# Performance work log

Hardware: AMD Instinct MI355X
Metric: run time of the kernel (lower is better)

## Reference

```python
import jax, jax.numpy as jnp
import numpy as np
import math

B, T, E, H = 2, 2048, 1024, 16
HD = E // H


def layernorm(x, g, b, eps=1e-5):
    mu = jnp.mean(x, axis=-1, keepdims=True)
    var = jnp.var(x, axis=-1, keepdims=True)
    return (x - mu) * jax.lax.rsqrt(var + eps) * g + b


def new_gelu(x):
    c = math.sqrt(2.0 / math.pi)
    return 0.5 * x * (1.0 + jnp.tanh(c * (x + 0.044715 * x ** 3)))


def setup_inputs() -> dict:
    key = jax.random.key(0)
    ks = jax.random.split(key, 6)
    s = 0.02
    return {
        "x": jax.random.normal(ks[0], (B, T, E), jnp.float32),
        "ln1_g": jnp.ones((E,), jnp.float32),
        "ln1_b": jnp.zeros((E,), jnp.float32),
        "w_attn": jax.random.normal(ks[1], (E, 3 * E), jnp.float32) * s,
        "b_attn": jnp.zeros((3 * E,), jnp.float32),
        "w_proj": jax.random.normal(ks[2], (E, E), jnp.float32) * s,
        "b_proj": jnp.zeros((E,), jnp.float32),
        "ln2_g": jnp.ones((E,), jnp.float32),
        "ln2_b": jnp.zeros((E,), jnp.float32),
        "w_fc": jax.random.normal(ks[3], (E, 4 * E), jnp.float32) * s,
        "b_fc": jnp.zeros((4 * E,), jnp.float32),
        "w_fc2": jax.random.normal(ks[4], (4 * E, E), jnp.float32) * s,
        "b_fc2": jnp.zeros((E,), jnp.float32),
    }


def reference(x, ln1_g, ln1_b, w_attn, b_attn, w_proj, b_proj,
              ln2_g, ln2_b, w_fc, b_fc, w_fc2, b_fc2):
    # --- attention branch (pre-norm) ---
    h = layernorm(x, ln1_g, ln1_b)
    qkv = h @ w_attn + b_attn                      # [B,T,3E]
    q, k, v = jnp.split(qkv, 3, axis=-1)
    # [B,T,E] -> [B,H,T,HD]
    q = q.reshape(B, T, H, HD).transpose(0, 2, 1, 3)
    k = k.reshape(B, T, H, HD).transpose(0, 2, 1, 3)
    v = v.reshape(B, T, H, HD).transpose(0, 2, 1, 3)
    att = jnp.einsum('bhqd,bhkd->bhqk', q, k) * (1.0 / math.sqrt(HD))
    causal = jnp.tril(jnp.ones((T, T), bool))       # [T,T]
    att = jnp.where(causal, att, -jnp.inf)
    att = jax.nn.softmax(att, axis=-1)
    y = jnp.einsum('bhqk,bhkd->bhqd', att, v)       # [B,H,T,HD]
    y = y.transpose(0, 2, 1, 3).reshape(B, T, E)
    y = y @ w_proj + b_proj
    x = x + y
    # --- MLP branch (pre-norm) ---
    h = layernorm(x, ln2_g, ln2_b)
    h = new_gelu(h @ w_fc + b_fc)
    h = h @ w_fc2 + b_fc2
    return x + h
```

## Files before the change

kernel.cpp:

```cpp
#include <hip/hip_runtime.h>

typedef unsigned short u16;
typedef unsigned int   u32;
typedef short bf16x8 __attribute__((ext_vector_type(8)));
typedef float f32x4  __attribute__((ext_vector_type(4)));

__device__ __forceinline__ float bf_lo(u32 u){ return __uint_as_float(u << 16); }
__device__ __forceinline__ float bf_hi(u32 u){ return __uint_as_float(u & 0xffff0000u); }
__device__ __forceinline__ u16 bf16r(float f){
  u32 u = __float_as_uint(f);
  u += 0x7fffu + ((u >> 16) & 1u);
  return (u16)(u >> 16);
}
__device__ __forceinline__ u32 pack2(float a, float b){
  return (u32)bf16r(a) | ((u32)bf16r(b) << 16);
}
__device__ __forceinline__ u32 pk_trunc(float a, float b){
  return (__float_as_uint(a) >> 16) | (__float_as_uint(b) & 0xffff0000u);
}
__device__ __forceinline__ float gelu_f(float x){
  float t = 0.7978845608028654f * (x + 0.044715f * x * x * x);
  t = fminf(fmaxf(t, -12.f), 12.f);
  float e = __expf(2.f * t);
  float th = (e - 1.f) / (e + 1.f);
  return 0.5f * x * (1.f + th);
}
__device__ __forceinline__ void glds16(const void* g, void* l) {
  __builtin_amdgcn_global_load_lds(
      (const __attribute__((address_space(1))) void*)g,
      (__attribute__((address_space(3))) void*)l, 16, 0, 0);
}

#define QSCALE 0.1803368801111204f

__device__ __forceinline__ void wt_body(const float* __restrict__ W,
                                        u16* __restrict__ Wt, int K, int N,
                                        int kx, int nx) {
  __shared__ float t[32][33];
  int k0 = kx * 32, n0 = nx * 32;
  int tx = threadIdx.x & 31, ty = threadIdx.x >> 5;
  #pragma unroll
  for (int i = 0; i < 32; i += 8)
    t[ty + i][tx] = W[(size_t)(k0 + ty + i) * N + n0 + tx];
  __syncthreads();
  #pragma unroll
  for (int i = 0; i < 32; i += 8)
    Wt[(size_t)(n0 + ty + i) * K + k0 + tx] = bf16r(t[tx][ty + i]);
}

__device__ __forceinline__ void ln_body(const float* __restrict__ x,
                                        const float* __restrict__ g,
                                        const float* __restrict__ bta,
                                        u16* __restrict__ out, int row) {
  int tid = threadIdx.x;
  const float4 xv = ((const float4*)(x + (size_t)row * 1024))[tid];
  float s = xv.x + xv.y + xv.z + xv.w;
  float q = xv.x*xv.x + xv.y*xv.y + xv.z*xv.z + xv.w*xv.w;
  #pragma unroll
  for (int off = 32; off > 0; off >>= 1) {
    s += __shfl_down(s, off);
    q += __shfl_down(q, off);
  }
  __shared__ float ss[4], sq[4];
  if ((tid & 63) == 0) { ss[tid >> 6] = s; sq[tid >> 6] = q; }
  __syncthreads();
  s = ss[0] + ss[1] + ss[2] + ss[3];
  q = sq[0] + sq[1] + sq[2] + sq[3];
  float mu = s * (1.f/1024.f);
  float rs = rsqrtf(q * (1.f/1024.f) - mu*mu + 1e-5f);
  const float4 gv = ((const float4*)g)[tid];
  const float4 bv = ((const float4*)bta)[tid];
  uint2 o;
  o.x = pack2((xv.x-mu)*rs*gv.x + bv.x, (xv.y-mu)*rs*gv.y + bv.y);
  o.y = pack2((xv.z-mu)*rs*gv.z + bv.z, (xv.w-mu)*rs*gv.w + bv.w);
  ((uint2*)(out + (size_t)row * 1024))[tid] = o;
}

__global__ __launch_bounds__(256) void prep_k(
    const float* __restrict__ w_attn, const float* __restrict__ w_proj,
    const float* __restrict__ w_fc,   const float* __restrict__ w_fc2,
    u16* __restrict__ wt_attn, u16* __restrict__ wt_proj,
    u16* __restrict__ wt_fc,   u16* __restrict__ wt_fc2,
    const float* __restrict__ x, const float* __restrict__ g,
    const float* __restrict__ b, u16* __restrict__ h1)
{
  int i = blockIdx.x;
  if (i < 3072)       wt_body(w_attn, wt_attn, 1024, 3072, i & 31, i >> 5);
  else if (i < 4096)  { int j = i - 3072; wt_body(w_proj, wt_proj, 1024, 1024, j & 31, j >> 5); }
  else if (i < 8192)  { int j = i - 4096; wt_body(w_fc,   wt_fc,   1024, 4096, j & 31, j >> 5); }
  else if (i < 12288) { int j = i - 8192; wt_body(w_fc2,  wt_fc2,  4096, 1024, j & 127, j >> 7); }
  else                ln_body(x, g, b, h1, i - 12288);
}

__global__ __launch_bounds__(256) void ln_k(const float* __restrict__ x,
                                            const float* __restrict__ g,
                                            const float* __restrict__ bta,
                                            u16* __restrict__ out) {
  ln_body(x, g, bta, out, blockIdx.x);
}

template<int MODE, int MI, int LB>
__global__ __launch_bounds__(256, LB) void gemm_k(
    const u16* __restrict__ A, const u16* __restrict__ Bt,
    const float* __restrict__ bias, const float* __restrict__ resid,
    void* __restrict__ out, int M, int N, int K, int lda,
    u16* __restrict__ vtb)
{
  constexpr int TM = MI * 32;
  __shared__ u16 Al[TM * 64];
  __shared__ u16 Bl[128 * 64];
  const int tid = threadIdx.x;
  const int by = blockIdx.y;
  const int sp = (MODE == 5) ? (by >> 3) : 0;
  const int n0 = (MODE == 5) ? ((by & 7) * 128) : (by * 128);
  const size_t koff = (size_t)sp * K;
  const int m0 = blockIdx.x * TM;
  const int wave = tid >> 6, lane = tid & 63;
  const int wm = (wave >> 1) * (MI * 16), wn = (wave & 1) * 64;
  const int l15 = lane & 15, quad = lane >> 4;
  const int sr = lane >> 3, cs = lane & 7;
  f32x4 acc[MI][4];
  const f32x4 zero = {0.f, 0.f, 0.f, 0.f};
  #pragma unroll
  for (int i = 0; i < MI; ++i)
    #pragma unroll
    for (int j = 0; j < 4; ++j)
      acc[i][j] = zero;
  for (int k0 = 0; k0 < K; k0 += 64) {
    __syncthreads();
    #pragma unroll
    for (int it = 0; it < MI; ++it) {
      int r = it*32 + wave*8 + sr;
      int c = cs ^ (r & 7);
      glds16(&A[(size_t)(m0 + r) * lda + koff + k0 + c*8], &Al[(it*32 + wave*8) * 64]);
    }
    #pragma unroll
    for (int it = 0; it < 4; ++it) {
      int r = it*32 + wave*8 + sr;
      int c = cs ^ (r & 7);
      glds16(&Bt[(size_t)(n0 + r) * lda + koff + k0 + c*8], &Bl[(it*32 + wave*8) * 64]);
    }
    __syncthreads();
    #pragma unroll
    for (int kk = 0; kk < 2; ++kk) {
      bf16x8 af[MI], bfr[4];
      #pragma unroll
      for (int i = 0; i < MI; ++i) {
        int R = wm + i*16 + l15;
        af[i] = *(const bf16x8*)&Al[R*64 + ((kk*4 + quad) ^ (R & 7)) * 8];
      }
      #pragma unroll
      for (int j = 0; j < 4; ++j) {
        int R = wn + j*16 + l15;
        bfr[j] = *(const bf16x8*)&Bl[R*64 + ((kk*4 + quad) ^ (R & 7)) * 8];
      }
      #pragma unroll
      for (int i = 0; i < MI; ++i)
        #pragma unroll
        for (int j = 0; j < 4; ++j)
          acc[i][j] = __builtin_amdgcn_mfma_f32_16x16x32_bf16(af[i], bfr[j], acc[i][j], 0, 0, 0);
    }
  }
  #pragma unroll
  for (int i = 0; i < MI; ++i) {
    #pragma unroll
    for (int j = 0; j < 4; ++j) {
      int col = n0 + wn + j*16 + l15;
      float bv = (MODE == 5) ? 0.f : bias[col];
      if constexpr (MODE == 4) {
        if (col >= 2048) {
          int t0 = m0 + wm + i*16 + quad*4;
          size_t vidx = ((size_t)((t0 >> 11)*1024 + (col - 2048)))*2048 + (t0 & 2047);
          uint2 pw;
          pw.x = pack2(acc[i][j][0] + bv, acc[i][j][1] + bv);
          pw.y = pack2(acc[i][j][2] + bv, acc[i][j][3] + bv);
          *(uint2*)&vtb[vidx] = pw;
          continue;
        }
      }
      float sc = (MODE == 4 && col < 1024) ? QSCALE : 1.0f;
      #pragma unroll
      for (int r = 0; r < 4; ++r) {
        int row = m0 + wm + i*16 + quad*4 + r;
        size_t idx = (size_t)row * N + col;
        float v = acc[i][j][r] + bv;
        if constexpr (MODE == 0)      ((u16*)out)[idx] = bf16r(v);
        else if constexpr (MODE == 1) ((float*)out)[idx] = v + resid[idx];
        else if constexpr (MODE == 2) ((u16*)out)[idx] = bf16r(gelu_f(v));
        else if constexpr (MODE == 4) ((u16*)out)[idx] = bf16r(v * sc);
        else if constexpr (MODE == 5) ((u16*)out)[(size_t)sp*M*N + idx] = bf16r(v);
        else                          ((float*)out)[idx] = v + resid[idx];
      }
    }
  }
}

__global__ __launch_bounds__(256) void cmb_k(const u16* __restrict__ p,
                                             const float* __restrict__ bias,
                                             const float* __restrict__ x2,
                                             float* __restrict__ out) {
  int row = blockIdx.x, t = threadIdx.x;
  size_t i = (size_t)row * 1024 + t*4;
  uint2 a = *(const uint2*)&p[i];
  uint2 b = *(const uint2*)&p[4194304 + i];
  float4 xv = ((const float4*)x2)[i >> 2];
  float4 bv = ((const float4*)bias)[t];
  float4 o;
  o.x = bf_lo(a.x) + bf_lo(b.x) + bv.x + xv.x;
  o.y = bf_hi(a.x) + bf_hi(b.x) + bv.y + xv.y;
  o.z = bf_lo(a.y) + bf_lo(b.y) + bv.z + xv.z;
  o.w = bf_hi(a.y) + bf_hi(b.y) + bv.w + xv.w;
  ((float4*)out)[i >> 2] = o;
}

__global__ __launch_bounds__(256, 4) void attn_k(const u16* __restrict__ qkv,
                                                 const u16* __restrict__ Vt,
                                                 u16* __restrict__ y) {
  __shared__ u16 Kl[64*64];
  __shared__ u16 Vl[64*64];
  __shared__ u16 Pw[4*16*72];
  const int tid = threadIdx.x;
  const int bh = blockIdx.x & 31, bb = bh >> 4, h = bh & 15;
  const int qt = 31 - (int)(blockIdx.x >> 5);
  const int w = tid >> 6, lane = tid & 63;
  const int l15 = lane & 15, quad = lane >> 4;
  const int sr = lane >> 3, cs = lane & 7;
  u16* Pme = Pw + w * (16*72);
  const int w16l = w*16 + l15;
  const int dquad = quad*4;

  const u16* qp = qkv + ((size_t)(bb*2048 + qt*64 + w16l))*3072 + h*64 + quad*8;
  const bf16x8 aq0 = *(const bf16x8*)qp;
  const bf16x8 aq1 = *(const bf16x8*)(qp + 32);

  f32x4 o[4];
  const f32x4 zero = {0.f,0.f,0.f,0.f};
  #pragma unroll
  for (int dt = 0; dt < 4; ++dt) o[dt] = zero;
  float l = 0.f;

  const u16* kbase = qkv + (size_t)bb*2048*3072 + 1024 + h*64;
  const u16* vbase = Vt + (size_t)bh*64*2048;

  for (int kt = 0; kt <= qt; ++kt) {
    __syncthreads();
    #pragma unroll
    for (int it = 0; it < 2; ++it) {
      int r = it*32 + w*8 + sr;
      int c = cs ^ (r & 7);
      glds16(kbase + (size_t)(kt*64 + r)*3072 + c*8, &Kl[(it*32 + w*8) * 64]);
      glds16(vbase + (size_t)r*2048 + kt*64 + c*8,   &Vl[(it*32 + w*8) * 64]);
    }
    __syncthreads();
    bf16x8 ak[4][2], av[4][2];
    #pragma unroll
    for (int nt = 0; nt < 4; ++nt) {
      int R = nt*16 + l15;
      #pragma unroll
      for (int kk = 0; kk < 2; ++kk) {
        ak[nt][kk] = *(const bf16x8*)&Kl[R*64 + ((kk*4 + quad) ^ (R & 7)) * 8];
        av[nt][kk] = *(const bf16x8*)&Vl[R*64 + ((kk*4 + quad) ^ (R & 7)) * 8];
      }
    }
    f32x4 sv[4];
    #pragma unroll
    for (int nt = 0; nt < 4; ++nt) {
      f32x4 s = zero;
      s = __builtin_amdgcn_mfma_f32_16x16x32_bf16(ak[nt][0], aq0, s, 0, 0, 0);
      s = __builtin_amdgcn_mfma_f32_16x16x32_bf16(ak[nt][1], aq1, s, 0, 0, 0);
      sv[nt] = s;
    }
    if (kt == qt) {
      #pragma unroll
      for (int nt = 0; nt < 4; ++nt)
        #pragma unroll
        for (int r = 0; r < 4; ++r)
          if (nt*16 + dquad + r > w16l) sv[nt][r] = -1e30f;
    }
    float pv[4][4];
    #pragma unroll
    for (int nt = 0; nt < 4; ++nt)
      #pragma unroll
      for (int r = 0; r < 4; ++r)
        pv[nt][r] = exp2f(sv[nt][r]);
    l += ((pv[0][0]+pv[0][1])+(pv[0][2]+pv[0][3]))
       + ((pv[1][0]+pv[1][1])+(pv[1][2]+pv[1][3]))
       + ((pv[2][0]+pv[2][1])+(pv[2][2]+pv[2][3]))
       + ((pv[3][0]+pv[3][1])+(pv[3][2]+pv[3][3]));
    #pragma unroll
    for (int nt = 0; nt < 4; ++nt) {
      uint2 pr;
      pr.x = pk_trunc(pv[nt][0], pv[nt][1]);
      pr.y = pk_trunc(pv[nt][2], pv[nt][3]);
      *(uint2*)&Pme[l15*72 + nt*16 + dquad] = pr;
    }
    const bf16x8 bp0 = *(const bf16x8*)&Pme[l15*72 + quad*8];
    const bf16x8 bp1 = *(const bf16x8*)&Pme[l15*72 + 32 + quad*8];
    #pragma unroll
    for (int dt = 0; dt < 4; ++dt) {
      o[dt] = __builtin_amdgcn_mfma_f32_16x16x32_bf16(av[dt][0], bp0, o[dt], 0, 0, 0);
      o[dt] = __builtin_amdgcn_mfma_f32_16x16x32_bf16(av[dt][1], bp1, o[dt], 0, 0, 0);
    }
  }
  float lt = l;
  lt += __shfl_xor(lt, 16);
  lt += __shfl_xor(lt, 32);
  float inv = 1.f / lt;
  u16* yp = y + ((size_t)(bb*2048 + qt*64 + w16l))*1024 + h*64;
  #pragma unroll
  for (int dt = 0; dt < 4; ++dt) {
    uint2 pk;
    pk.x = pack2(o[dt][0]*inv, o[dt][1]*inv);
    pk.y = pack2(o[dt][2]*inv, o[dt][3]*inv);
    *(uint2*)(yp + dt*16 + dquad) = pk;
  }
}

extern "C" void kernel_launch(void* const* d_in, const int* in_sizes, int n_in,
                              void* d_out, int out_size, void* d_ws, size_t ws_size,
                              hipStream_t stream) {
  const float* x      = (const float*)d_in[0];
  const float* ln1_g  = (const float*)d_in[1];
  const float* ln1_b  = (const float*)d_in[2];
  const float* w_attn = (const float*)d_in[3];
  const float* b_attn = (const float*)d_in[4];
  const float* w_proj = (const float*)d_in[5];
  const float* b_proj = (const float*)d_in[6];
  const float* ln2_g  = (const float*)d_in[7];
  const float* ln2_b  = (const float*)d_in[8];
  const float* w_fc   = (const float*)d_in[9];
  const float* b_fc   = (const float*)d_in[10];
  const float* w_fc2  = (const float*)d_in[11];
  const float* b_fc2  = (const float*)d_in[12];

  char* ws = (char*)d_ws;
  u16*   wt_attn = (u16*)(ws);
  u16*   wt_proj = (u16*)(ws + 6291456);
  u16*   wt_fc   = (u16*)(ws + 8388608);
  u16*   wt_fc2  = (u16*)(ws + 16777216);
  u16*   h1      = (u16*)(ws + 25165824);
  u16*   qkvb    = (u16*)(ws + 33554432);
  u16*   yb      = (u16*)(ws + 58720256);
  float* x2      = (float*)(ws + 67108864);
  u16*   h2  = h1;
  u16*   vtb = (u16*)(ws + 67108864);
  u16*   act = qkvb;
  u16*   pk2 = (u16*)(ws);

  prep_k<<<dim3(16384), 256, 0, stream>>>(w_attn, w_proj, w_fc, w_fc2,
                                          wt_attn, wt_proj, wt_fc, wt_fc2,
                                          x, ln1_g, ln1_b, h1);
  gemm_k<4,4,3><<<dim3(32, 24), 256, 0, stream>>>(h1, wt_attn, b_attn, nullptr,
      (void*)qkvb, 4096, 3072, 1024, 1024, vtb);
  attn_k<<<dim3(1024), 256, 0, stream>>>(qkvb, vtb, yb);
  gemm_k<1,2,3><<<dim3(64, 8), 256, 0, stream>>>(yb, wt_proj, b_proj, x,
      (void*)x2, 4096, 1024, 1024, 1024, nullptr);
  ln_k<<<4096, 256, 0, stream>>>(x2, ln2_g, ln2_b, h2);
  gemm_k<2,4,3><<<dim3(32, 32), 256, 0, stream>>>(h2, wt_fc, b_fc, nullptr,
      (void*)act, 4096, 4096, 1024, 1024, nullptr);
  gemm_k<5,2,3><<<dim3(64, 16), 256, 0, stream>>>(act, wt_fc2, b_fc2, nullptr,
      (void*)pk2, 4096, 1024, 2048, 4096, nullptr);
  cmb_k<<<4096, 256, 0, stream>>>(pk2, b_fc2, x2, (float*)d_out);
}
```

Measured before the change: 311.3 us.

## Add 256x256 8-wave ping-pong GEMM kernel for QKV and FC1

```diff
diff --git a/kernel.cpp b/kernel.cpp
--- a/kernel.cpp
+++ b/kernel.cpp
@@ -167,18 +167,6 @@
     for (int j = 0; j < 4; ++j) {
       int col = n0 + wn + j*16 + l15;
       float bv = (MODE == 5) ? 0.f : bias[col];
-      if constexpr (MODE == 4) {
-        if (col >= 2048) {
-          int t0 = m0 + wm + i*16 + quad*4;
-          size_t vidx = ((size_t)((t0 >> 11)*1024 + (col - 2048)))*2048 + (t0 & 2047);
-          uint2 pw;
-          pw.x = pack2(acc[i][j][0] + bv, acc[i][j][1] + bv);
-          pw.y = pack2(acc[i][j][2] + bv, acc[i][j][3] + bv);
-          *(uint2*)&vtb[vidx] = pw;
-          continue;
-        }
-      }
-      float sc = (MODE == 4 && col < 1024) ? QSCALE : 1.0f;
       #pragma unroll
       for (int r = 0; r < 4; ++r) {
         int row = m0 + wm + i*16 + quad*4 + r;
@@ -187,12 +175,140 @@
         if constexpr (MODE == 0)      ((u16*)out)[idx] = bf16r(v);
         else if constexpr (MODE == 1) ((float*)out)[idx] = v + resid[idx];
         else if constexpr (MODE == 2) ((u16*)out)[idx] = bf16r(gelu_f(v));
-        else if constexpr (MODE == 4) ((u16*)out)[idx] = bf16r(v * sc);
         else if constexpr (MODE == 5) ((u16*)out)[(size_t)sp*M*N + idx] = bf16r(v);
         else                          ((float*)out)[idx] = v + resid[idx];
       }
     }
   }
+}
+
+#define BAR8 __builtin_amdgcn_s_barrier()
+#define VM4  asm volatile("s_waitcnt vmcnt(4)" ::: "memory")
+
+template<int MODE>
+__global__ __launch_bounds__(512, 2) void gemm8_k(
+    const u16* __restrict__ A, const u16* __restrict__ Bt,
+    const float* __restrict__ bias, void* __restrict__ out,
+    int M, int N, int K, int lda, u16* __restrict__ vtb)
+{
+  __shared__ u16 Al[2][256*64];
+  __shared__ u16 Bl[2][256*64];
+  const int tid = threadIdx.x;
+  const int m0 = blockIdx.x * 256;
+  const int n0 = blockIdx.y * 256;
+  const int wave = tid >> 6, lane = tid & 63;
+  const int wm = wave >> 2, wn = wave & 3;
+  const int l15 = lane & 15, quad = lane >> 4;
+  const int srow = tid >> 3;
+  const int scl  = (tid & 7) ^ (srow & 7);
+  const int NT = K >> 6;
+
+  const u16* pA = A  + (size_t)(m0 + srow) * lda + scl * 8;
+  const u16* pB = Bt + (size_t)(n0 + srow) * lda + scl * 8;
+
+  f32x4 acc[2][2][4][2];
+  const f32x4 zero = {0.f,0.f,0.f,0.f};
+  #pragma unroll
+  for (int a = 0; a < 2; ++a)
+    #pragma unroll
+    for (int b = 0; b < 2; ++b)
+      #pragma unroll
+      for (int c = 0; c < 4; ++c)
+        #pragma unroll
+        for (int d = 0; d < 2; ++d) acc[a][b][c][d] = zero;
+
+  bf16x8 afr[4][2];
+  bf16x8 bfr[2][2][2];
+
+#define STG_A(b,h,t) do { \
+    glds16(pA + ((h)*128      ) * lda + (t)*64, &Al[b][((h)*128      + wave*8) * 64]); \
+    glds16(pA + ((h)*128 + 64 ) * lda + (t)*64, &Al[b][((h)*128 + 64 + wave*8) * 64]); } while(0)
+#define STG_B(b,h,t) do { \
+    glds16(pB + ((h)*128      ) * lda + (t)*64, &Bl[b][((h)*128      + wave*8) * 64]); \
+    glds16(pB + ((h)*128 + 64 ) * lda + (t)*64, &Bl[b][((h)*128 + 64 + wave*8) * 64]); } while(0)
+#define RD_A(b,qm) do { _Pragma("unroll") \
+    for (int mi = 0; mi < 4; ++mi) { \
+      int R = (qm)*128 + wm*64 + mi*16 + l15; \
+      afr[mi][0] = *(const bf16x8*)&Al[b][R*64 + ((quad     ^ (l15 & 7)) * 8)]; \
+      afr[mi][1] = *(const bf16x8*)&Al[b][R*64 + (((4+quad) ^ (l15 & 7)) * 8)]; } } while(0)
+#define RD_B(b,qn) do { _Pragma("unroll") \
+    for (int ni = 0; ni < 2; ++ni) { \
+      int R = (qn)*128 + wn*32 + ni*16 + l15; \
+      bfr[qn][ni][0] = *(const bf16x8*)&Bl[b][R*64 + ((quad     ^ (l15 & 7)) * 8)]; \
+      bfr[qn][ni][1] = *(const bf16x8*)&Bl[b][R*64 + (((4+quad) ^ (l15 & 7)) * 8)]; } } while(0)
+#define MM(qm,qn) do { __builtin_amdgcn_s_setprio(1); _Pragma("unroll") \
+    for (int mi = 0; mi < 4; ++mi) { _Pragma("unroll") \
+      for (int ni = 0; ni < 2; ++ni) { \
+        acc[qm][qn][mi][ni] = __builtin_amdgcn_mfma_f32_16x16x32_bf16(afr[mi][0], bfr[qn][ni][0], acc[qm][qn][mi][ni], 0, 0, 0); \
+        acc[qm][qn][mi][ni] = __builtin_amdgcn_mfma_f32_16x16x32_bf16(afr[mi][1], bfr[qn][ni][1], acc[qm][qn][mi][ni], 0, 0, 0); } } \
+    __builtin_amdgcn_s_setprio(0); } while(0)
+
+  STG_A(0,0,0); STG_B(0,0,0); STG_A(0,1,0); STG_B(0,1,0);
+  STG_A(1,0,1); STG_B(1,0,1);
+  VM4; BAR8;
+
+  const int NI = NT >> 1;
+  for (int j = 0; j < NI; ++j) {
+    const int t1 = 2*j + 1;
+    const int t2 = (2*j + 2 < NT) ? 2*j + 2 : NT - 1;
+    const int t3 = (2*j + 3 < NT) ? 2*j + 3 : NT - 1;
+    RD_A(0,0); RD_B(0,0); STG_A(1,1,t1);
+    BAR8; MM(0,0); BAR8;
+    RD_B(0,1); STG_B(1,1,t1);
+    BAR8; MM(0,1); BAR8;
+    RD_A(0,1); STG_A(0,0,t2);
+    BAR8; MM(1,0); BAR8;
+    STG_B(0,0,t2);
+    BAR8; MM(1,1); VM4; BAR8;
+    RD_A(1,0); RD_B(1,0); STG_A(0,1,t2);
+    BAR8; MM(0,0); BAR8;
+    RD_B(1,1); STG_B(0,1,t2);
+    BAR8; MM(0,1); BAR8;
+    RD_A(1,1); STG_A(1,0,t3);
+    BAR8; MM(1,0); BAR8;
+    STG_B(1,0,t3);
+    BAR8; MM(1,1); VM4; BAR8;
+  }
+
+  #pragma unroll
+  for (int qm = 0; qm < 2; ++qm) {
+    #pragma unroll
+    for (int qn = 0; qn < 2; ++qn) {
+      #pragma unroll
+      for (int mi = 0; mi < 4; ++mi) {
+        #pragma unroll
+        for (int ni = 0; ni < 2; ++ni) {
+          const int col  = n0 + qn*128 + wn*32 + ni*16 + l15;
+          const int rowb = m0 + qm*128 + wm*64 + mi*16 + quad*4;
+          const float bv = bias[col];
+          const f32x4 v = acc[qm][qn][mi][ni];
+          if constexpr (MODE == 4) {
+            if (col >= 2048) {
+              uint2 pw;
+              pw.x = pack2(v[0] + bv, v[1] + bv);
+              pw.y = pack2(v[2] + bv, v[3] + bv);
+              size_t vidx = ((size_t)((rowb >> 11)*1024 + (col - 2048)))*2048 + (rowb & 2047);
+              *(uint2*)&vtb[vidx] = pw;
+              continue;
+            }
+            const float sc = (col < 1024) ? QSCALE : 1.0f;
+            #pragma unroll
+            for (int r = 0; r < 4; ++r)
+              ((u16*)out)[(size_t)(rowb + r) * N + col] = bf16r((v[r] + bv) * sc);
+          } else {
+            #pragma unroll
+            for (int r = 0; r < 4; ++r)
+              ((u16*)out)[(size_t)(rowb + r) * N + col] = bf16r(gelu_f(v[r] + bv));
+          }
+        }
+      }
+    }
+  }
+#undef STG_A
+#undef STG_B
+#undef RD_A
+#undef RD_B
+#undef MM
 }
 
 __global__ __launch_bounds__(256) void cmb_k(const u16* __restrict__ p,
@@ -350,15 +466,15 @@
   prep_k<<<dim3(16384), 256, 0, stream>>>(w_attn, w_proj, w_fc, w_fc2,
                                           wt_attn, wt_proj, wt_fc, wt_fc2,
                                           x, ln1_g, ln1_b, h1);
-  gemm_k<4,4,3><<<dim3(32, 24), 256, 0, stream>>>(h1, wt_attn, b_attn, nullptr,
+  gemm8_k<4><<<dim3(16, 12), 512, 0, stream>>>(h1, wt_attn, b_attn,
       (void*)qkvb, 4096, 3072, 1024, 1024, vtb);
   attn_k<<<dim3(1024), 256, 0, stream>>>(qkvb, vtb, yb);
   gemm_k<1,2,3><<<dim3(64, 8), 256, 0, stream>>>(yb, wt_proj, b_proj, x,
       (void*)x2, 4096, 1024, 1024, 1024, nullptr);
   ln_k<<<4096, 256, 0, stream>>>(x2, ln2_g, ln2_b, h2);
-  gemm_k<2,4,3><<<dim3(32, 32), 256, 0, stream>>>(h2, wt_fc, b_fc, nullptr,
+  gemm8_k<2><<<dim3(16, 16), 512, 0, stream>>>(h2, wt_fc, b_fc,
       (void*)act, 4096, 4096, 1024, 1024, nullptr);
-  gemm_k<5,2,3><<<dim3(64, 16), 256, 0, stream>>>(act, wt_fc2, b_fc2, nullptr,
+  gemm_k<5,4,3><<<dim3(32, 16), 256, 0, stream>>>(act, wt_fc2, b_fc2, nullptr,
       (void*)pk2, 4096, 1024, 2048, 4096, nullptr);
   cmb_k<<<4096, 256, 0, stream>>>(pk2, b_fc2, x2, (float*)d_out);
 }
```

Result: no change. 314.6 us (+1.1%).
